# Optimization experiments

Measured on AMD Instinct MI355X. Metric: run time of the kernel, lower is better.

The kernel has to match this reference:

```python
import jax, jax.numpy as jnp
import numpy as np

N_USER = 60000
N_ITEM = 120000
N = N_USER + N_ITEM
EMB = 64
LAYERS = [64, 64, 64]
BATCH = 4096
NNZ_ADJ = 3_600_000
NNZ_UG = 960_000
NNZ_IG = 1_920_000


def spmm(rows, cols, vals, x, n_rows):
    # sparse (COO) @ dense: out[r] += v * x[c]
    return jax.ops.segment_sum(vals[:, None] * x[cols], rows, num_segments=n_rows)


def l2_normalize(x, eps=1e-12):
    n = jnp.linalg.norm(x, axis=1, keepdims=True)
    return x / jnp.maximum(n, eps)


def setup_inputs() -> dict:
    key = jax.random.key(0)
    ks = jax.random.split(key, 24)
    s = 0.1  # xavier-like init scale for 64-dim fan
    inp = {
        'users': jax.random.randint(ks[0], (BATCH,), 0, N_USER),
        'pos_items': jax.random.randint(ks[1], (BATCH,), 0, N_ITEM),
        'neg_items': jax.random.randint(ks[2], (BATCH,), 0, N_ITEM),
        # normalized bipartite adjacency (COO)
        'adj_rows': jax.random.randint(ks[3], (NNZ_ADJ,), 0, N),
        'adj_cols': jax.random.randint(ks[4], (NNZ_ADJ,), 0, N),
        'adj_vals': jax.random.uniform(ks[5], (NNZ_ADJ,), jnp.float32) * 0.05,
        # user-user graph for user_GNN
        'ug_rows': jax.random.randint(ks[6], (NNZ_UG,), 0, N_USER),
        'ug_cols': jax.random.randint(ks[7], (NNZ_UG,), 0, N_USER),
        'ug_vals': jax.random.uniform(ks[8], (NNZ_UG,), jnp.float32) * 0.06,
        # item-item graph for item_GNN
        'ig_rows': jax.random.randint(ks[9], (NNZ_IG,), 0, N_ITEM),
        'ig_cols': jax.random.randint(ks[10], (NNZ_IG,), 0, N_ITEM),
        'ig_vals': jax.random.uniform(ks[11], (NNZ_IG,), jnp.float32) * 0.06,
        'user_emb': jax.random.normal(ks[12], (N_USER, EMB), jnp.float32) * s,
        'item_emb': jax.random.normal(ks[13], (N_ITEM, EMB), jnp.float32) * s,
        # NGCF propagation weights, stacked over 3 layers (all 64x64)
        'W_gc': jax.random.normal(ks[14], (3, EMB, EMB), jnp.float32) * s,
        'b_gc': jax.random.normal(ks[15], (3, 1, EMB), jnp.float32) * s,
        'W_bi': jax.random.normal(ks[16], (3, EMB, EMB), jnp.float32) * s,
        'b_bi': jax.random.normal(ks[17], (3, 1, EMB), jnp.float32) * s,
        # 2-layer GCN weights for user/item side graphs
        'Wu0': jax.random.normal(ks[18], (EMB, 64), jnp.float32) * s,
        'bu0': jnp.zeros((64,), jnp.float32),
        'Wu1': jax.random.normal(ks[19], (64, 64), jnp.float32) * s,
        'bu1': jnp.zeros((64,), jnp.float32),
        'Wi0': jax.random.normal(ks[20], (EMB, 64), jnp.float32) * s,
        'bi0': jnp.zeros((64,), jnp.float32),
        'Wi1': jax.random.normal(ks[21], (64, 64), jnp.float32) * s,
        'bi1': jnp.zeros((64,), jnp.float32),
    }
    return inp


def reference(users, pos_items, neg_items,
              adj_rows, adj_cols, adj_vals,
              ug_rows, ug_cols, ug_vals,
              ig_rows, ig_cols, ig_vals,
              user_emb, item_emb,
              W_gc, b_gc, W_bi, b_bi,
              Wu0, bu0, Wu1, bu1, Wi0, bi0, Wi1, bi1):
    # side GCNs on user-user / item-item graphs (2 GraphConv layers, elu between)
    u_h = jax.nn.elu(spmm(ug_rows, ug_cols, ug_vals, user_emb, N_USER) @ Wu0 + bu0)
    u_h = spmm(ug_rows, ug_cols, ug_vals, u_h, N_USER) @ Wu1 + bu1
    i_h = jax.nn.elu(spmm(ig_rows, ig_cols, ig_vals, item_emb, N_ITEM) @ Wi0 + bi0)
    i_h = spmm(ig_rows, ig_cols, ig_vals, i_h, N_ITEM) @ Wi1 + bi1

    # NGCF propagation on the bipartite graph
    ego = jnp.concatenate([user_emb, item_emb], axis=0)  # [N, 64]
    all_emb = [ego]
    for k in range(len(LAYERS)):
        side = spmm(adj_rows, adj_cols, adj_vals, ego, N)         # [N, 64]
        sum_e = side @ W_gc[k] + b_gc[k]
        bi_e = (ego * side) @ W_bi[k] + b_bi[k]
        ego = jax.nn.leaky_relu(sum_e + bi_e, negative_slope=0.2)
        all_emb.append(l2_normalize(ego))
    all_emb = jnp.concatenate(all_emb, axis=1)  # [N, 256]

    u_g = all_emb[:N_USER]
    i_g = all_emb[N_USER:]

    # in-place relu in the torch code mutates the GNN outputs before concat
    user_full = jnp.concatenate([u_g, jax.nn.relu(u_h)], axis=1)  # [N_USER, 320]
    item_full = jnp.concatenate([i_g, jax.nn.relu(i_h)], axis=1)  # [N_ITEM, 320]

    return (user_full[users], item_full[pos_items], item_full[neg_items])
```

## Files before the change

kernel.cpp:

```cpp
#include <hip/hip_runtime.h>
#include <hip/hip_bf16.h>

#define N_USER 60000
#define N_ITEM 120000
#define NTOT   180000
#define NNZ_ADJ 3600000
#define NNZ_UG   960000
#define NNZ_IG  1920000

#define RSB     2048
#define NSB_ADJ ((NTOT  + RSB - 1) / RSB)
#define NSB_UG  ((N_USER+ RSB - 1) / RSB)
#define NSB_IG  ((N_ITEM+ RSB - 1) / RSB)
#define CAPA_SB 43008
#define CAPU_SB 34816
#define CAPI_SB 34816
#define CHUNK   4096
#define PB_U ((NNZ_UG  + CHUNK - 1) / CHUNK)
#define PB_I ((NNZ_IG  + CHUNK - 1) / CHUNK)
#define PB_A ((NNZ_ADJ + CHUNK - 1) / CHUNK)

typedef __hip_bfloat16 bf16;
typedef __attribute__((ext_vector_type(8))) short bf16x8;
typedef __attribute__((ext_vector_type(4))) float f32x4;

__device__ __forceinline__ float ldf(const void* p, long i, int f) {
    return f ? ((const float*)p)[i] : __bfloat162float(((const bf16*)p)[i]);
}

__device__ __forceinline__ unsigned pk2(float a, float b) {
    unsigned short lo = __bfloat16_as_ushort(__float2bfloat16(a));
    unsigned short hi = __bfloat16_as_ushort(__float2bfloat16(b));
    return (unsigned)lo | ((unsigned)hi << 16);
}

__device__ __forceinline__ bf16x8 mul_bf8(bf16x8 x, bf16x8 y) {
    bf16x8 r;
#pragma unroll
    for (int e = 0; e < 8; e++) {
        float xf = __uint_as_float(((unsigned)(unsigned short)x[e]) << 16);
        float yf = __uint_as_float(((unsigned)(unsigned short)y[e]) << 16);
        r[e] = (short)__bfloat16_as_ushort(__float2bfloat16(xf * yf));
    }
    return r;
}

__global__ void k_detect(const void* __restrict__ vals, int* __restrict__ flag) {
    if (threadIdx.x == 0 && blockIdx.x == 0) {
        const unsigned short* w = (const unsigned short*)vals;
        int cnt = 0;
        for (int i = 0; i < 512; i += 2) cnt += (w[i] >> 15) & 1;
        *flag = (cnt > 16) ? 1 : 0;
    }
}

__global__ __launch_bounds__(256) void k_cast16(const void* __restrict__ ue,
                                                const void* __restrict__ ie,
                                                bf16* __restrict__ ego16,
                                                const int* __restrict__ flag) {
    int f = *flag;
    long i = (long)blockIdx.x * 256 + threadIdx.x;
    const long uN = (long)N_USER * 64;
    if (i < (long)NTOT * 64) {
        float v = (i < uN) ? ldf(ue, i, f) : ldf(ie, i - uN, f);
        ego16[i] = __float2bfloat16(v);
    }
}

__global__ void k_initpos3(int* __restrict__ sbU, int* __restrict__ sbI,
                           int* __restrict__ sbA) {
    int i = threadIdx.x;
    if (i < NSB_UG)  sbU[i * 16] = i * CAPU_SB;
    if (i < NSB_IG)  sbI[i * 16] = i * CAPI_SB;
    if (i < NSB_ADJ) sbA[i * 16] = i * CAPA_SB;
}

__global__ __launch_bounds__(256) void k_part3(const int* __restrict__ rU, const int* __restrict__ cU, const void* __restrict__ vU,
                                               const int* __restrict__ rI, const int* __restrict__ cI, const void* __restrict__ vI,
                                               const int* __restrict__ rA, const int* __restrict__ cA, const void* __restrict__ vA,
                                               uint2* __restrict__ recU, uint2* __restrict__ recI, uint2* __restrict__ recA,
                                               int* __restrict__ sbU, int* __restrict__ sbI, int* __restrict__ sbA,
                                               const int* __restrict__ flag) {
    __shared__ int lcnt[96];
    __shared__ int lbase[96];
    int f = *flag;
    int t = threadIdx.x;
    int b = blockIdx.x;
    const int *rows, *cols; const void* vals; uint2* rec; int* sbpos; int nnz, base;
    if (b < PB_U)             { rows = rU; cols = cU; vals = vU; rec = recU; sbpos = sbU; nnz = NNZ_UG;  base = b * CHUNK; }
    else if (b < PB_U + PB_I) { rows = rI; cols = cI; vals = vI; rec = recI; sbpos = sbI; nnz = NNZ_IG;  base = (b - PB_U) * CHUNK; }
    else                      { rows = rA; cols = cA; vals = vA; rec = recA; sbpos = sbA; nnz = NNZ_ADJ; base = (b - PB_U - PB_I) * CHUNK; }

    if (t < 96) lcnt[t] = 0;
    __syncthreads();
#pragma unroll
    for (int k = 0; k < CHUNK / 256; k += 4) {
        int e0 = base + k * 256 + t;
        int e1 = e0 + 256, e2 = e0 + 512, e3 = e0 + 768;
        int s0 = (e0 < nnz) ? (rows[e0] >> 11) : -1;
        int s1 = (e1 < nnz) ? (rows[e1] >> 11) : -1;
        int s2 = (e2 < nnz) ? (rows[e2] >> 11) : -1;
        int s3 = (e3 < nnz) ? (rows[e3] >> 11) : -1;
        if (s0 >= 0) atomicAdd(&lcnt[s0], 1);
        if (s1 >= 0) atomicAdd(&lcnt[s1], 1);
        if (s2 >= 0) atomicAdd(&lcnt[s2], 1);
        if (s3 >= 0) atomicAdd(&lcnt[s3], 1);
    }
    __syncthreads();
    if (t < 96) {
        int c = lcnt[t];
        lbase[t] = c ? atomicAdd(&sbpos[t * 16], c) : 0;
        lcnt[t] = 0;
    }
    __syncthreads();
#pragma unroll
    for (int k = 0; k < CHUNK / 256; k += 4) {
        int e0 = base + k * 256 + t;
        int e1 = e0 + 256, e2 = e0 + 512, e3 = e0 + 768;
        bool g0 = e0 < nnz, g1 = e1 < nnz, g2 = e2 < nnz, g3 = e3 < nnz;
        int r0 = g0 ? rows[e0] : 0;
        int r1 = g1 ? rows[e1] : 0;
        int r2 = g2 ? rows[e2] : 0;
        int r3 = g3 ? rows[e3] : 0;
        int c0 = g0 ? cols[e0] : 0;
        int c1 = g1 ? cols[e1] : 0;
        int c2 = g2 ? cols[e2] : 0;
        int c3 = g3 ? cols[e3] : 0;
        float v0 = g0 ? ldf(vals, e0, f) : 0.0f;
        float v1 = g1 ? ldf(vals, e1, f) : 0.0f;
        float v2 = g2 ? ldf(vals, e2, f) : 0.0f;
        float v3 = g3 ? ldf(vals, e3, f) : 0.0f;
        if (g0) { int sb = r0 >> 11; int o = atomicAdd(&lcnt[sb], 1);
                  rec[lbase[sb] + o] = make_uint2(((unsigned)(r0 & 2047) << 18) | (unsigned)c0, __float_as_uint(v0)); }
        if (g1) { int sb = r1 >> 11; int o = atomicAdd(&lcnt[sb], 1);
                  rec[lbase[sb] + o] = make_uint2(((unsigned)(r1 & 2047) << 18) | (unsigned)c1, __float_as_uint(v1)); }
        if (g2) { int sb = r2 >> 11; int o = atomicAdd(&lcnt[sb], 1);
                  rec[lbase[sb] + o] = make_uint2(((unsigned)(r2 & 2047) << 18) | (unsigned)c2, __float_as_uint(v2)); }
        if (g3) { int sb = r3 >> 11; int o = atomicAdd(&lcnt[sb], 1);
                  rec[lbase[sb] + o] = make_uint2(((unsigned)(r3 & 2047) << 18) | (unsigned)c3, __float_as_uint(v3)); }
    }
}

__global__ __launch_bounds__(1024) void k_sortsb3(
        const uint2* __restrict__ recU, uint2* __restrict__ rec2U, int* __restrict__ rstartU, int* __restrict__ rendU, const int* __restrict__ sbU,
        const uint2* __restrict__ recI, uint2* __restrict__ rec2I, int* __restrict__ rstartI, int* __restrict__ rendI, const int* __restrict__ sbI,
        const uint2* __restrict__ recA, uint2* __restrict__ rec2A, int* __restrict__ rstartA, int* __restrict__ rendA, const int* __restrict__ sbA) {
    __shared__ int cnt[RSB];
    __shared__ int pos[RSB];
    __shared__ int wsum[16];
    int b = blockIdx.x, t = threadIdx.x;
    const uint2* rec; uint2* rec2; int* rstart; int* rend; const int* sbpos;
    int cap, n_rows, lb;
    if (b < NSB_UG) {
        lb = b; rec = recU; rec2 = rec2U; rstart = rstartU; rend = rendU;
        sbpos = sbU; cap = CAPU_SB; n_rows = N_USER;
    } else if (b < NSB_UG + NSB_IG) {
        lb = b - NSB_UG; rec = recI; rec2 = rec2I; rstart = rstartI; rend = rendI;
        sbpos = sbI; cap = CAPI_SB; n_rows = N_ITEM;
    } else {
        lb = b - NSB_UG - NSB_IG; rec = recA; rec2 = rec2A; rstart = rstartA; rend = rendA;
        sbpos = sbA; cap = CAPA_SB; n_rows = NTOT;
    }
    int s = lb * cap;
    int e = sbpos[lb * 16];
    cnt[t] = 0; cnt[t + 1024] = 0;
    __syncthreads();
    int j = s + t;
    for (; j + 3072 < e; j += 4096) {
        uint2 r0 = rec[j];
        uint2 r1 = rec[j + 1024];
        uint2 r2 = rec[j + 2048];
        uint2 r3 = rec[j + 3072];
        atomicAdd(&cnt[r0.x >> 18], 1);
        atomicAdd(&cnt[r1.x >> 18], 1);
        atomicAdd(&cnt[r2.x >> 18], 1);
        atomicAdd(&cnt[r3.x >> 18], 1);
    }
    for (; j < e; j += 1024)
        atomicAdd(&cnt[rec[j].x >> 18], 1);
    __syncthreads();
    int a  = cnt[2 * t];
    int bb = cnt[2 * t + 1];
    int ps = a + bb;
    int incl = ps;
    int lane = t & 63;
#pragma unroll
    for (int d = 1; d < 64; d <<= 1) {
        int v = __shfl_up(incl, d, 64);
        if (lane >= d) incl += v;
    }
    int wv = t >> 6;
    if (lane == 63) wsum[wv] = incl;
    __syncthreads();
    if (t < 16) {
        int v  = wsum[t];
        int iv = v;
#pragma unroll
        for (int d = 1; d < 16; d <<= 1) {
            int w = __shfl_up(iv, d, 64);
            if (t >= d) iv += w;
        }
        wsum[t] = iv - v;
    }
    __syncthreads();
    int ex0 = wsum[wv] + (incl - ps);
    pos[2 * t]     = ex0;
    pos[2 * t + 1] = ex0 + a;
    int row0 = lb * RSB;
    {
        int ra = row0 + 2 * t;
        if (ra < n_rows) { rstart[ra] = s + ex0;      rend[ra] = s + ex0 + a; }
        int rb = ra + 1;
        if (rb < n_rows) { rstart[rb] = s + ex0 + a;  rend[rb] = s + ex0 + a + bb; }
    }
    __syncthreads();
    j = s + t;
    for (; j + 3072 < e; j += 4096) {
        uint2 r0 = rec[j];
        uint2 r1 = rec[j + 1024];
        uint2 r2 = rec[j + 2048];
        uint2 r3 = rec[j + 3072];
        int o0 = atomicAdd(&pos[r0.x >> 18], 1);
        int o1 = atomicAdd(&pos[r1.x >> 18], 1);
        int o2 = atomicAdd(&pos[r2.x >> 18], 1);
        int o3 = atomicAdd(&pos[r3.x >> 18], 1);
        rec2[s + o0] = r0;
        rec2[s + o1] = r1;
        rec2[s + o2] = r2;
        rec2[s + o3] = r3;
    }
    for (; j < e; j += 1024) {
        uint2 r = rec[j];
        int o = atomicAdd(&pos[r.x >> 18], 1);
        rec2[s + o] = r;
    }
}

#define ACC8(q, v)                                      \
    a[0] += (v) * __uint_as_float((q).x << 16);         \
    a[1] += (v) * __uint_as_float((q).x & 0xFFFF0000u); \
    a[2] += (v) * __uint_as_float((q).y << 16);         \
    a[3] += (v) * __uint_as_float((q).y & 0xFFFF0000u); \
    a[4] += (v) * __uint_as_float((q).z << 16);         \
    a[5] += (v) * __uint_as_float((q).z & 0xFFFF0000u); \
    a[6] += (v) * __uint_as_float((q).w << 16);         \
    a[7] += (v) * __uint_as_float((q).w & 0xFFFF0000u);

__device__ __forceinline__ void spmm_row(int row, int p,
                                         const int* __restrict__ rstart,
                                         const int* __restrict__ rend,
                                         const uint2* __restrict__ rec,
                                         const bf16* __restrict__ x,
                                         bf16* __restrict__ out) {
    int s = rstart[row], e = rend[row];
    const uint4* xb = (const uint4*)x;
    float a[8];
#pragma unroll
    for (int i = 0; i < 8; i++) a[i] = 0.0f;

    int j = s;
    for (; j + 4 <= e; j += 4) {
        uint2 r0 = rec[j];
        uint2 r1 = rec[j + 1];
        uint2 r2 = rec[j + 2];
        uint2 r3 = rec[j + 3];
        uint4 q0 = xb[(long)(r0.x & 0x3FFFF) * 8 + p];
        uint4 q1 = xb[(long)(r1.x & 0x3FFFF) * 8 + p];
        uint4 q2 = xb[(long)(r2.x & 0x3FFFF) * 8 + p];
        uint4 q3 = xb[(long)(r3.x & 0x3FFFF) * 8 + p];
        float v0 = __uint_as_float(r0.y);
        float v1 = __uint_as_float(r1.y);
        float v2 = __uint_as_float(r2.y);
        float v3 = __uint_as_float(r3.y);
        ACC8(q0, v0)
        ACC8(q1, v1)
        ACC8(q2, v2)
        ACC8(q3, v3)
    }
    for (; j < e; j++) {
        uint2 r = rec[j];
        uint4 q = xb[(long)(r.x & 0x3FFFF) * 8 + p];
        float v = __uint_as_float(r.y);
        ACC8(q, v)
    }

    *(uint4*)(out + (long)row * 64 + p * 8) =
        make_uint4(pk2(a[0], a[1]), pk2(a[2], a[3]),
                   pk2(a[4], a[5]), pk2(a[6], a[7]));
}

__global__ __launch_bounds__(256) void k_spmm_bf(const int* __restrict__ rstart,
                                                 const int* __restrict__ rend,
                                                 const uint2* __restrict__ rec,
                                                 const bf16* __restrict__ x,
                                                 bf16* __restrict__ out,
                                                 int n_rows) {
    int row = blockIdx.x * 32 + (threadIdx.x >> 3);
    int p = threadIdx.x & 7;
    if (row >= n_rows) return;
    spmm_row(row, p, rstart, rend, rec, x, out);
}

__global__ __launch_bounds__(256) void k_spmm2(
        const int* __restrict__ rs0, const int* __restrict__ re0, const uint2* __restrict__ rc0,
        const bf16* __restrict__ x0, bf16* __restrict__ o0, int n0, int nb0,
        const int* __restrict__ rs1, const int* __restrict__ re1, const uint2* __restrict__ rc1,
        const bf16* __restrict__ x1, bf16* __restrict__ o1, int n1) {
    int b = blockIdx.x;
    int p = threadIdx.x & 7;
    int rl = threadIdx.x >> 3;
    if (b < nb0) {
        int row = b * 32 + rl;
        if (row < n0) spmm_row(row, p, rs0, re0, rc0, x0, o0);
    } else {
        int row = (b - nb0) * 32 + rl;
        if (row < n1) spmm_row(row, p, rs1, re1, rc1, x1, o1);
    }
}

template <int ACT>
__global__ __launch_bounds__(256) void k_gemm2(
        const bf16* __restrict__ X0, const void* __restrict__ W0, const void* __restrict__ b0,
        bf16* __restrict__ Y0, int M0, int nb0,
        const bf16* __restrict__ X1, const void* __restrict__ W1, const void* __restrict__ b1,
        bf16* __restrict__ Y1, int M1,
        const int* __restrict__ flag) {
    __shared__ bf16 WtH[64][72];
    __shared__ bf16 WtL[64][72];
    __shared__ float bl[64];
    int f = *flag;
    int tid = threadIdx.x;
    int bId = blockIdx.x;
    const bf16* X; const void* W; const void* bb; bf16* Y; int M, sb, nbseg;
    if (bId < nb0) { X = X0; W = W0; bb = b0; Y = Y0; M = M0; sb = bId; nbseg = nb0; }
    else { X = X1; W = W1; bb = b1; Y = Y1; M = M1; sb = bId - nb0; nbseg = gridDim.x - nb0; }

    for (int idx = tid; idx < 4096; idx += 256) {
        int n = idx >> 6, kk = idx & 63;
        float v = ldf(W, (long)kk * 64 + n, f);
        bf16 h = __float2bfloat16(v);
        WtH[n][kk] = h;
        WtL[n][kk] = __float2bfloat16(v - __bfloat162float(h));
    }
    if (tid < 64) bl[tid] = ldf(bb, tid, f);
    __syncthreads();

    int l  = tid & 63;
    int lr = l & 15;
    int lk = l >> 4;

    bf16x8 bh[2][4], bbf[2][4];
#pragma unroll
    for (int kt = 0; kt < 2; kt++)
#pragma unroll
        for (int ct = 0; ct < 4; ct++) {
            int n  = ct * 16 + lr;
            int ko = kt * 32 + lk * 8;
            bh[kt][ct]  = *(const bf16x8*)&WtH[n][ko];
            bbf[kt][ct] = *(const bf16x8*)&WtL[n][ko];
        }

    int nt  = M >> 4;
    int wid = sb * 4 + (tid >> 6);
    int nw  = nbseg * 4;

    for (int t = wid; t < nt; t += nw) {
        const bf16* Ap = X + (long)(t * 16 + lr) * 64 + lk * 8;
        bf16x8 a[2];
#pragma unroll
        for (int kt = 0; kt < 2; kt++) a[kt] = *(const bf16x8*)(Ap + kt * 32);

        f32x4 acc[4];
#pragma unroll
        for (int ct = 0; ct < 4; ct++) {
            float bv = bl[ct * 16 + lr];
            acc[ct] = (f32x4){bv, bv, bv, bv};
        }
#pragma unroll
        for (int kt = 0; kt < 2; kt++)
#pragma unroll
            for (int ct = 0; ct < 4; ct++) {
                acc[ct] = __builtin_amdgcn_mfma_f32_16x16x32_bf16(a[kt], bh[kt][ct], acc[ct], 0, 0, 0);
                acc[ct] = __builtin_amdgcn_mfma_f32_16x16x32_bf16(a[kt], bbf[kt][ct], acc[ct], 0, 0, 0);
            }

#pragma unroll
        for (int r = 0; r < 4; r++) {
            float v0 = acc[0][r], v1 = acc[1][r], v2 = acc[2][r], v3 = acc[3][r];
            if (ACT == 2) {
                v0 = fmaxf(v0, 0.0f); v1 = fmaxf(v1, 0.0f);
                v2 = fmaxf(v2, 0.0f); v3 = fmaxf(v3, 0.0f);
            } else {
                v0 = (v0 > 0.0f) ? v0 : (expf(v0) - 1.0f);
                v1 = (v1 > 0.0f) ? v1 : (expf(v1) - 1.0f);
                v2 = (v2 > 0.0f) ? v2 : (expf(v2) - 1.0f);
                v3 = (v3 > 0.0f) ? v3 : (expf(v3) - 1.0f);
            }
            long ob = (long)(t * 16 + lk * 4 + r) * 64 + lr;
            Y[ob]      = __float2bfloat16(v0);
            Y[ob + 16] = __float2bfloat16(v1);
            Y[ob + 32] = __float2bfloat16(v2);
            Y[ob + 48] = __float2bfloat16(v3);
        }
    }
}

__global__ __launch_bounds__(256) void k_layer(const bf16* __restrict__ S,
                                               const bf16* __restrict__ Ein,
                                               bf16* __restrict__ Eout,
                                               const void* __restrict__ Wgc,
                                               const void* __restrict__ bgc,
                                               const void* __restrict__ Wbi,
                                               const void* __restrict__ bbi,
                                               long woff, long boff,
                                               float* __restrict__ scale, int M,
                                               const int* __restrict__ flag) {
    __shared__ bf16 W1H[64][72];
    __shared__ bf16 W1L[64][72];
    __shared__ bf16 W2H[64][72];
    __shared__ bf16 W2L[64][72];
    __shared__ float bl[64];
    int f = *flag;
    int tid = threadIdx.x;
    for (int idx = tid; idx < 4096; idx += 256) {
        int n = idx >> 6, kk = idx & 63;
        float v1 = ldf(Wgc, woff + (long)kk * 64 + n, f);
        float v2 = ldf(Wbi, woff + (long)kk * 64 + n, f);
        bf16 h1 = __float2bfloat16(v1);
        bf16 h2 = __float2bfloat16(v2);
        W1H[n][kk] = h1;
        W1L[n][kk] = __float2bfloat16(v1 - __bfloat162float(h1));
        W2H[n][kk] = h2;
        W2L[n][kk] = __float2bfloat16(v2 - __bfloat162float(h2));
    }
    if (tid < 64) bl[tid] = ldf(bgc, boff + tid, f) + ldf(bbi, boff + tid, f);
    __syncthreads();

    int l  = tid & 63;
    int lr = l & 15;
    int lk = l >> 4;

    bf16x8 w1h[2][4], w1l[2][4], w2h[2][4], w2l[2][4];
#pragma unroll
    for (int kt = 0; kt < 2; kt++)
#pragma unroll
        for (int ct = 0; ct < 4; ct++) {
            int n  = ct * 16 + lr;
            int ko = kt * 32 + lk * 8;
            w1h[kt][ct] = *(const bf16x8*)&W1H[n][ko];
            w1l[kt][ct] = *(const bf16x8*)&W1L[n][ko];
            w2h[kt][ct] = *(const bf16x8*)&W2H[n][ko];
            w2l[kt][ct] = *(const bf16x8*)&W2L[n][ko];
        }

    int nt  = M >> 4;
    int wid = blockIdx.x * 4 + (tid >> 6);
    int nw  = gridDim.x * 4;

    for (int t = wid; t < nt; t += nw) {
        long rb = (long)(t * 16 + lr) * 64 + lk * 8;
        bf16x8 sv[2], pv[2];
        sv[0] = *(const bf16x8*)(S + rb);
        sv[1] = *(const bf16x8*)(S + rb + 32);
        {
            bf16x8 e0 = *(const bf16x8*)(Ein + rb);
            bf16x8 e1 = *(const bf16x8*)(Ein + rb + 32);
            pv[0] = mul_bf8(e0, sv[0]);
            pv[1] = mul_bf8(e1, sv[1]);
        }

        f32x4 acc[4];
#pragma unroll
        for (int ct = 0; ct < 4; ct++) {
            float bv = bl[ct * 16 + lr];
            acc[ct] = (f32x4){bv, bv, bv, bv};
        }
#pragma unroll
        for (int kt = 0; kt < 2; kt++)
#pragma unroll
            for (int ct = 0; ct < 4; ct++) {
                acc[ct] = __builtin_amdgcn_mfma_f32_16x16x32_bf16(sv[kt], w1h[kt][ct], acc[ct], 0, 0, 0);
                acc[ct] = __builtin_amdgcn_mfma_f32_16x16x32_bf16(sv[kt], w1l[kt][ct], acc[ct], 0, 0, 0);
                acc[ct] = __builtin_amdgcn_mfma_f32_16x16x32_bf16(pv[kt], w2h[kt][ct], acc[ct], 0, 0, 0);
                acc[ct] = __builtin_amdgcn_mfma_f32_16x16x32_bf16(pv[kt], w2l[kt][ct], acc[ct], 0, 0, 0);
            }

#pragma unroll
        for (int r = 0; r < 4; r++) {
            float v0 = acc[0][r], v1 = acc[1][r], v2 = acc[2][r], v3 = acc[3][r];
            v0 = (v0 > 0.0f) ? v0 : 0.2f * v0;
            v1 = (v1 > 0.0f) ? v1 : 0.2f * v1;
            v2 = (v2 > 0.0f) ? v2 : 0.2f * v2;
            v3 = (v3 > 0.0f) ? v3 : 0.2f * v3;
            float ss = v0 * v0 + v1 * v1 + v2 * v2 + v3 * v3;
            ss += __shfl_xor(ss, 1, 64);
            ss += __shfl_xor(ss, 2, 64);
            ss += __shfl_xor(ss, 4, 64);
            ss += __shfl_xor(ss, 8, 64);
            float sc2 = 1.0f / fmaxf(sqrtf(ss), 1e-12f);
            int grow = t * 16 + lk * 4 + r;
            long ob = (long)grow * 64 + lr;
            Eout[ob]      = __float2bfloat16(v0);
            Eout[ob + 16] = __float2bfloat16(v1);
            Eout[ob + 32] = __float2bfloat16(v2);
            Eout[ob + 48] = __float2bfloat16(v3);
            if (lr == 0) scale[grow] = sc2;
        }
    }
}

__global__ __launch_bounds__(64) void k_gather(const int* __restrict__ users,
                                               const int* __restrict__ pos,
                                               const int* __restrict__ neg,
                                               const void* __restrict__ ue,
                                               const void* __restrict__ ie,
                                               const bf16* __restrict__ E1,
                                               const bf16* __restrict__ E2,
                                               const bf16* __restrict__ E3,
                                               const float* __restrict__ s1,
                                               const float* __restrict__ s2,
                                               const float* __restrict__ s3,
                                               const bf16* __restrict__ uh,
                                               const bf16* __restrict__ ih,
                                               void* __restrict__ out,
                                               const int* __restrict__ flag) {
    int f = *flag;
    int b = blockIdx.x;
    int which = b >> 12;
    int s = b & 4095;
    int lane = threadIdx.x;
    long ebase, nrow;
    const void* e0;
    const bf16* hh;
    if (which == 0) {
        int r = users[s];
        e0 = ue; ebase = (long)r * 64;
        hh = uh + (long)r * 64;
        nrow = (long)r;
    } else {
        int r = (which == 1) ? pos[s] : neg[s];
        e0 = ie; ebase = (long)r * 64;
        hh = ih + (long)r * 64;
        nrow = (long)(N_USER + r);
    }
    long nbase = nrow * 64;
    float o0 = ldf(e0, ebase + lane, f);
    float o1 = __bfloat162float(E1[nbase + lane]) * s1[nrow];
    float o2 = __bfloat162float(E2[nbase + lane]) * s2[nrow];
    float o3 = __bfloat162float(E3[nbase + lane]) * s3[nrow];
    float o4 = __bfloat162float(hh[lane]);
    long ob = (long)b * 320;
    if (f) {
        float* o = (float*)out + ob;
        o[lane] = o0; o[64 + lane] = o1; o[128 + lane] = o2;
        o[192 + lane] = o3; o[256 + lane] = o4;
    } else {
        bf16* o = (bf16*)out + ob;
        o[lane]       = __float2bfloat16(o0);
        o[64 + lane]  = __float2bfloat16(o1);
        o[128 + lane] = __float2bfloat16(o2);
        o[192 + lane] = __float2bfloat16(o3);
        o[256 + lane] = __float2bfloat16(o4);
    }
}

extern "C" void kernel_launch(void* const* d_in, const int* in_sizes, int n_in,
                              void* d_out, int out_size, void* d_ws, size_t ws_size,
                              hipStream_t stream) {
    const int* users = (const int*)d_in[0];
    const int* pos   = (const int*)d_in[1];
    const int* neg   = (const int*)d_in[2];
    const int* adj_r = (const int*)d_in[3];
    const int* adj_c = (const int*)d_in[4];
    const void* adj_v = d_in[5];
    const int* ug_r  = (const int*)d_in[6];
    const int* ug_c  = (const int*)d_in[7];
    const void* ug_v = d_in[8];
    const int* ig_r  = (const int*)d_in[9];
    const int* ig_c  = (const int*)d_in[10];
    const void* ig_v = d_in[11];
    const void* ue   = d_in[12];
    const void* ie   = d_in[13];
    const void* Wgc  = d_in[14];
    const void* bgc  = d_in[15];
    const void* Wbi  = d_in[16];
    const void* bbi  = d_in[17];
    const void* Wu0  = d_in[18];
    const void* bu0  = d_in[19];
    const void* Wu1  = d_in[20];
    const void* bu1  = d_in[21];
    const void* Wi0  = d_in[22];
    const void* bi0  = d_in[23];
    const void* Wi1  = d_in[24];
    const void* bi1  = d_in[25];

    char* ws = (char*)d_ws;
    int*   FLAG  = (int*)(ws + 0);
    bf16*  S16A  = (bf16*)(ws + 256);
    uint2* recTmpA = (uint2*)(ws + 256);
    bf16*  SU    = (bf16*)(ws + 30277888L);
    bf16*  SI    = (bf16*)(ws + 46080256L);
    bf16*  ego16 = (bf16*)(ws + 61440256L);
    bf16*  UH    = (bf16*)(ws + 84480256L);
    bf16*  IH    = (bf16*)(ws + 92160256L);
    bf16*  E1    = (bf16*)(ws + 107520256L);
    bf16*  E2    = (bf16*)(ws + 130560256L);
    bf16*  E3    = (bf16*)(ws + 153600256L);
    uint2* recTmpU = (uint2*)(ws + 130560256L);
    bf16*  TI    = (bf16*)(ws + 130560256L);
    bf16*  TU    = (bf16*)(ws + 145920256L);
    uint2* recTmpI = (uint2*)(ws + 153600256L);
    uint2* rec2A = (uint2*)(ws + 176640256L);
    uint2* rec2U = (uint2*)(ws + 206917888L);
    uint2* rec2I = (uint2*)(ws + 215273728L);
    int* rstartA = (int*)(ws + 231706880L);
    int* rendA   = (int*)(ws + 232426880L);
    int* rstartU = (int*)(ws + 233146880L);
    int* rendU   = (int*)(ws + 233386880L);
    int* rstartI = (int*)(ws + 233626880L);
    int* rendI   = (int*)(ws + 234106880L);
    int* sbposU  = (int*)(ws + 234586880L);
    int* sbposI  = (int*)(ws + 234588928L);
    int* sbposA  = (int*)(ws + 234593024L);
    float* SC1   = (float*)(ws + 234600192L);
    float* SC2   = (float*)(ws + 235320192L);
    float* SC3   = (float*)(ws + 236040192L);

    k_detect<<<1, 64, 0, stream>>>(adj_v, FLAG);
    k_cast16<<<45000, 256, 0, stream>>>(ue, ie, ego16, FLAG);

    k_initpos3<<<1, 256, 0, stream>>>(sbposU, sbposI, sbposA);
    k_part3<<<PB_U + PB_I + PB_A, 256, 0, stream>>>(ug_r, ug_c, ug_v,
                                                    ig_r, ig_c, ig_v,
                                                    adj_r, adj_c, adj_v,
                                                    recTmpU, recTmpI, recTmpA,
                                                    sbposU, sbposI, sbposA, FLAG);
    k_sortsb3<<<NSB_UG + NSB_IG + NSB_ADJ, 1024, 0, stream>>>(
        recTmpU, rec2U, rstartU, rendU, sbposU,
        recTmpI, rec2I, rstartI, rendI, sbposI,
        recTmpA, rec2A, rstartA, rendA, sbposA);

    const bf16* ego16I = ego16 + (size_t)N_USER * 64;
    int nbU = (N_USER + 31) / 32;
    int nbI = (N_ITEM + 31) / 32;
    int gu = (N_USER / 16 + 7) / 8;
    int gi = (N_ITEM / 16 + 7) / 8;
    k_spmm2<<<nbU + nbI, 256, 0, stream>>>(rstartU, rendU, rec2U, ego16,  SU, N_USER, nbU,
                                           rstartI, rendI, rec2I, ego16I, SI, N_ITEM);
    k_gemm2<1><<<gu + gi, 256, 0, stream>>>(SU, Wu0, bu0, TU, N_USER, gu,
                                            SI, Wi0, bi0, TI, N_ITEM, FLAG);
    k_spmm2<<<nbU + nbI, 256, 0, stream>>>(rstartU, rendU, rec2U, TU, SU, N_USER, nbU,
                                           rstartI, rendI, rec2I, TI, SI, N_ITEM);
    k_gemm2<2><<<gu + gi, 256, 0, stream>>>(SU, Wu1, bu1, UH, N_USER, gu,
                                            SI, Wi1, bi1, IH, N_ITEM, FLAG);

    bf16* Ebuf[4]  = {ego16, E1, E2, E3};
    float* SCs[3]  = {SC1, SC2, SC3};
    for (int k = 0; k < 3; k++) {
        k_spmm_bf<<<(NTOT + 31) / 32, 256, 0, stream>>>(rstartA, rendA, rec2A, Ebuf[k], S16A, NTOT);
        k_layer<<<704, 256, 0, stream>>>(S16A, Ebuf[k], Ebuf[k + 1],
                                         Wgc, bgc, Wbi, bbi,
                                         (long)k * 4096, (long)k * 64,
                                         SCs[k], NTOT, FLAG);
    }

    k_gather<<<12288, 64, 0, stream>>>(users, pos, neg, ue, ie, E1, E2, E3,
                                       SC1, SC2, SC3, UH, IH, d_out, FLAG);
}
```

Measured before the change: 818.8 us.

## Stage partition records in LDS for coalesced bucket writes and vectorized loads

The partition kernel now loads 16 consecutive rows, cols and vals per thread with vector loads, reading each input once instead of twice. It computes a local prefix sum of the bucket counts and scatters records into a shared-memory staging buffer grouped by bucket. The records are then written to global memory contiguously per bucket, replacing scattered 8-byte stores. In exchange it uses about 36KB of LDS per block, which may lower occupancy, and adds extra barriers and a scan.

```diff
diff --git a/kernel.cpp b/kernel.cpp
--- a/kernel.cpp
+++ b/kernel.cpp
@@ -82,7 +82,13 @@
                                                int* __restrict__ sbU, int* __restrict__ sbI, int* __restrict__ sbA,
                                                const int* __restrict__ flag) {
     __shared__ int lcnt[96];
+    __shared__ int lstart[96];
+    __shared__ int lpos[96];
     __shared__ int lbase[96];
+    __shared__ int wtmp;
+    __shared__ uint2 stage[CHUNK];
+    __shared__ unsigned char sbin[CHUNK];
+
     int f = *flag;
     int t = threadIdx.x;
     int b = blockIdx.x;
@@ -92,52 +98,91 @@
     else                      { rows = rA; cols = cA; vals = vA; rec = recA; sbpos = sbA; nnz = NNZ_ADJ; base = (b - PB_U - PB_I) * CHUNK; }
 
     if (t < 96) lcnt[t] = 0;
-    __syncthreads();
-#pragma unroll
-    for (int k = 0; k < CHUNK / 256; k += 4) {
-        int e0 = base + k * 256 + t;
-        int e1 = e0 + 256, e2 = e0 + 512, e3 = e0 + 768;
-        int s0 = (e0 < nnz) ? (rows[e0] >> 11) : -1;
-        int s1 = (e1 < nnz) ? (rows[e1] >> 11) : -1;
-        int s2 = (e2 < nnz) ? (rows[e2] >> 11) : -1;
-        int s3 = (e3 < nnz) ? (rows[e3] >> 11) : -1;
-        if (s0 >= 0) atomicAdd(&lcnt[s0], 1);
-        if (s1 >= 0) atomicAdd(&lcnt[s1], 1);
-        if (s2 >= 0) atomicAdd(&lcnt[s2], 1);
-        if (s3 >= 0) atomicAdd(&lcnt[s3], 1);
-    }
-    __syncthreads();
+
+    int base16 = base + t * 16;
+    int rr[16], cc[16];
+    float vv[16];
+    if (base + CHUNK <= nnz) {
+#pragma unroll
+        for (int k = 0; k < 4; k++) {
+            int4 r4 = *(const int4*)(rows + base16 + 4 * k);
+            int4 c4 = *(const int4*)(cols + base16 + 4 * k);
+            rr[4 * k + 0] = r4.x; rr[4 * k + 1] = r4.y; rr[4 * k + 2] = r4.z; rr[4 * k + 3] = r4.w;
+            cc[4 * k + 0] = c4.x; cc[4 * k + 1] = c4.y; cc[4 * k + 2] = c4.z; cc[4 * k + 3] = c4.w;
+        }
+        if (f) {
+#pragma unroll
+            for (int k = 0; k < 4; k++) {
+                float4 v4 = *(const float4*)((const float*)vals + base16 + 4 * k);
+                vv[4 * k + 0] = v4.x; vv[4 * k + 1] = v4.y; vv[4 * k + 2] = v4.z; vv[4 * k + 3] = v4.w;
+            }
+        } else {
+            const unsigned short* vb = (const unsigned short*)vals;
+#pragma unroll
+            for (int h = 0; h < 2; h++) {
+                uint4 q = *(const uint4*)(vb + base16 + 8 * h);
+                vv[8 * h + 0] = __uint_as_float(q.x << 16);
+                vv[8 * h + 1] = __uint_as_float(q.x & 0xFFFF0000u);
+                vv[8 * h + 2] = __uint_as_float(q.y << 16);
+                vv[8 * h + 3] = __uint_as_float(q.y & 0xFFFF0000u);
+                vv[8 * h + 4] = __uint_as_float(q.z << 16);
+                vv[8 * h + 5] = __uint_as_float(q.z & 0xFFFF0000u);
+                vv[8 * h + 6] = __uint_as_float(q.w << 16);
+                vv[8 * h + 7] = __uint_as_float(q.w & 0xFFFF0000u);
+            }
+        }
+    } else {
+#pragma unroll
+        for (int k = 0; k < 16; k++) {
+            int e = base16 + k;
+            if (e < nnz) { rr[k] = rows[e]; cc[k] = cols[e]; vv[k] = ldf(vals, e, f); }
+            else         { rr[k] = -1; cc[k] = 0; vv[k] = 0.0f; }
+        }
+    }
+    __syncthreads();
+
+#pragma unroll
+    for (int k = 0; k < 16; k++)
+        if (rr[k] >= 0) atomicAdd(&lcnt[rr[k] >> 11], 1);
+    __syncthreads();
+
+    int v = (t < 96) ? lcnt[t] : 0;
+    int incl = v;
+    {
+        int lane = t & 63;
+#pragma unroll
+        for (int d = 1; d < 64; d <<= 1) {
+            int w = __shfl_up(incl, d, 64);
+            if (lane >= d) incl += w;
+        }
+    }
+    if (t == 63) wtmp = incl;
+    __syncthreads();
+    if (t >= 64 && t < 96) incl += wtmp;
     if (t < 96) {
-        int c = lcnt[t];
-        lbase[t] = c ? atomicAdd(&sbpos[t * 16], c) : 0;
-        lcnt[t] = 0;
-    }
-    __syncthreads();
-#pragma unroll
-    for (int k = 0; k < CHUNK / 256; k += 4) {
-        int e0 = base + k * 256 + t;
-        int e1 = e0 + 256, e2 = e0 + 512, e3 = e0 + 768;
-        bool g0 = e0 < nnz, g1 = e1 < nnz, g2 = e2 < nnz, g3 = e3 < nnz;
-        int r0 = g0 ? rows[e0] : 0;
-        int r1 = g1 ? rows[e1] : 0;
-        int r2 = g2 ? rows[e2] : 0;
-        int r3 = g3 ? rows[e3] : 0;
-        int c0 = g0 ? cols[e0] : 0;
-        int c1 = g1 ? cols[e1] : 0;
-        int c2 = g2 ? cols[e2] : 0;
-        int c3 = g3 ? cols[e3] : 0;
-        float v0 = g0 ? ldf(vals, e0, f) : 0.0f;
-        float v1 = g1 ? ldf(vals, e1, f) : 0.0f;
-        float v2 = g2 ? ldf(vals, e2, f) : 0.0f;
-        float v3 = g3 ? ldf(vals, e3, f) : 0.0f;
-        if (g0) { int sb = r0 >> 11; int o = atomicAdd(&lcnt[sb], 1);
-                  rec[lbase[sb] + o] = make_uint2(((unsigned)(r0 & 2047) << 18) | (unsigned)c0, __float_as_uint(v0)); }
-        if (g1) { int sb = r1 >> 11; int o = atomicAdd(&lcnt[sb], 1);
-                  rec[lbase[sb] + o] = make_uint2(((unsigned)(r1 & 2047) << 18) | (unsigned)c1, __float_as_uint(v1)); }
-        if (g2) { int sb = r2 >> 11; int o = atomicAdd(&lcnt[sb], 1);
-                  rec[lbase[sb] + o] = make_uint2(((unsigned)(r2 & 2047) << 18) | (unsigned)c2, __float_as_uint(v2)); }
-        if (g3) { int sb = r3 >> 11; int o = atomicAdd(&lcnt[sb], 1);
-                  rec[lbase[sb] + o] = make_uint2(((unsigned)(r3 & 2047) << 18) | (unsigned)c3, __float_as_uint(v3)); }
+        int ex = incl - v;
+        lstart[t] = ex;
+        lpos[t]   = ex;
+        lbase[t]  = v ? atomicAdd(&sbpos[t * 16], v) : 0;
+    }
+    __syncthreads();
+
+#pragma unroll
+    for (int k = 0; k < 16; k++) {
+        if (rr[k] >= 0) {
+            int sb = rr[k] >> 11;
+            int o = atomicAdd(&lpos[sb], 1);
+            stage[o] = make_uint2(((unsigned)(rr[k] & 2047) << 18) | (unsigned)cc[k],
+                                  __float_as_uint(vv[k]));
+            sbin[o] = (unsigned char)sb;
+        }
+    }
+    __syncthreads();
+
+    int total = lstart[95] + lcnt[95];
+    for (int i = t; i < total; i += 256) {
+        int sb = sbin[i];
+        rec[lbase[sb] + (i - lstart[sb])] = stage[i];
     }
 }
 
```

Result: faster. 765.9 us (-6.5%).
